# Kernel optimization log

Measured on AMD Instinct MI355X. Metric: run time of the kernel, lower is better.

Reference implementation:

```python
import jax, jax.numpy as jnp
import numpy as np

H = 256    # hidden_size
CVQ = 64   # vq_ph_channel
K = 128    # vq_ph_codebook_dim
NL = 5     # num_layers per ConvBlocks
NB = 2     # layers_in_block
KS = 3     # kernel_size


def _ln_c(x, g, b, eps=1e-5):
    # LayerNorm over channel dim of a [B, C, T] tensor
    m = jnp.mean(x, axis=1, keepdims=True)
    v = jnp.mean((x - m) ** 2, axis=1, keepdims=True)
    return (x - m) * jax.lax.rsqrt(v + eps) * g[None, :, None] + b[None, :, None]


def _causal_conv(x, w, b):
    # x [B,Cin,T], w [Cout,Cin,K]; left (causal) padding of K-1
    y = jax.lax.conv_general_dilated(x, w, (1,), [(w.shape[-1] - 1, 0)],
                                     dimension_numbers=('NCH', 'OIH', 'NCH'))
    return y + b[None, :, None]


def _pw(x, w, b):
    # pointwise (kernel-size-1) conv: w [Cout, Cin]
    return jnp.einsum('oi,bit->bot', w, x) + b[None, :, None]


def _conv_blocks(x, mask, ln_g, ln_b, w1, b1, w2, b2, last_g, last_b, post_w, post_b):
    # LeftPadConvBlocks: NL residual blocks x NB sub-blocks of
    # LN -> causal conv (C->2C, k=3) -> *k^-0.5 -> GELU -> 1x1 conv (2C->C), residual + mask
    scale = KS ** -0.5
    for i in range(NL):
        for j in range(NB):
            h = _ln_c(x, ln_g[i, j], ln_b[i, j])
            h = _causal_conv(h, w1[i, j], b1[i, j]) * scale
            h = jax.nn.gelu(h, approximate=False)
            h = _pw(h, w2[i, j], b2[i, j])
            x = (x + h) * mask
    x = _ln_c(x, last_g, last_b) * mask
    x = _causal_conv(x, post_w, post_b) * mask
    return x


def _group_by_segs(h_bct, mel2ph, L):
    # scatter-mean mel frames into phoneme segments; index 0 = padding (dropped)
    h = jnp.swapaxes(h_bct, 1, 2)  # [B, T, H]
    def one(hb, mb):
        s = jnp.zeros((L + 1, hb.shape[-1]), hb.dtype).at[mb].add(hb)
        c = jnp.zeros((L + 1,), hb.dtype).at[mb].add(1.0)
        return s[1:] / jnp.clip(c[1:], 1.0)[:, None]
    g = jax.vmap(one)(h, mel2ph)   # [B, L, H]
    return jnp.swapaxes(g, 1, 2)   # [B, H, L]


def _vq(z, codebook, beta=0.25):
    # EMA-VQ forward math: nearest-codebook lookup + straight-through + commitment loss
    x = jnp.swapaxes(z, 1, 2)                                # [B, T, C]
    d = (jnp.sum(x ** 2, -1, keepdims=True)
         - 2.0 * jnp.einsum('btc,kc->btk', x, codebook)
         + jnp.sum(codebook ** 2, -1))                       # [B, T, K]
    idx = jnp.argmin(d, axis=-1)                             # [B, T]
    q = codebook[idx]                                        # [B, T, C]
    loss = beta * jnp.mean((x - jax.lax.stop_gradient(q)) ** 2)
    q_st = x + jax.lax.stop_gradient(q - x)
    return jnp.swapaxes(q_st, 1, 2), loss, idx


def setup_inputs() -> dict:
    key = jax.random.key(0)
    ks = list(jax.random.split(key, 64))
    it = iter(ks)
    B, T, L = 16, 2048, 512
    f = lambda shape, s: jax.random.normal(next(it), shape, jnp.float32) * s
    inp = {}
    inp['x'] = jax.random.normal(next(it), (B, 80, T), jnp.float32)
    inp['in_nonpadding'] = jnp.ones((B, 1, T), jnp.float32)
    inp['in_mel2ph'] = jnp.sort(jax.random.randint(next(it), (B, T), 1, L + 1), axis=-1)
    inp['ph_nonpadding'] = jnp.ones((B, 1, L), jnp.float32)
    inp['conv_in_w'] = f((H, 80), 0.05)
    inp['conv_in_b'] = jnp.zeros((H,), jnp.float32)
    for p in ('enc', 'pn'):
        inp[p + '_ln_g'] = jnp.ones((NL, NB, H), jnp.float32)
        inp[p + '_ln_b'] = jnp.zeros((NL, NB, H), jnp.float32)
        inp[p + '_w1'] = f((NL, NB, 2 * H, H, KS), 0.03)
        inp[p + '_b1'] = jnp.zeros((NL, NB, 2 * H), jnp.float32)
        inp[p + '_w2'] = f((NL, NB, H, 2 * H), 0.03)
        inp[p + '_b2'] = jnp.zeros((NL, NB, H), jnp.float32)
        inp[p + '_last_g'] = jnp.ones((H,), jnp.float32)
        inp[p + '_last_b'] = jnp.zeros((H,), jnp.float32)
        inp[p + '_post_w'] = f((H, H, KS), 0.03)
        inp[p + '_post_b'] = jnp.zeros((H,), jnp.float32)
    inp['proj_in_w'] = f((CVQ, H), 0.05)
    inp['proj_in_b'] = jnp.zeros((CVQ,), jnp.float32)
    inp['proj_out_w'] = f((H, CVQ), 0.05)
    inp['proj_out_b'] = jnp.zeros((H,), jnp.float32)
    inp['codebook'] = f((K, CVQ), 0.1)
    return inp


def reference(x, in_nonpadding, in_mel2ph, ph_nonpadding,
              conv_in_w, conv_in_b,
              enc_ln_g, enc_ln_b, enc_w1, enc_b1, enc_w2, enc_b2,
              enc_last_g, enc_last_b, enc_post_w, enc_post_b,
              pn_ln_g, pn_ln_b, pn_w1, pn_b1, pn_w2, pn_b2,
              pn_last_g, pn_last_b, pn_post_w, pn_post_b,
              proj_in_w, proj_in_b, proj_out_w, proj_out_b, codebook):
    L = ph_nonpadding.shape[-1]
    h = _pw(x, conv_in_w, conv_in_b) * in_nonpadding                     # ph_conv_in
    h = _conv_blocks(h, in_nonpadding, enc_ln_g, enc_ln_b, enc_w1, enc_b1,
                     enc_w2, enc_b2, enc_last_g, enc_last_b,
                     enc_post_w, enc_post_b) * in_nonpadding             # ph_encoder
    h = _group_by_segs(h, in_mel2ph, L)                                  # [B, H, L]
    h = _conv_blocks(h, ph_nonpadding, pn_ln_g, pn_ln_b, pn_w1, pn_b1,
                     pn_w2, pn_b2, pn_last_g, pn_last_b,
                     pn_post_w, pn_post_b) * ph_nonpadding               # ph_postnet
    z = _pw(h, proj_in_w, proj_in_b)                                     # ph_latents_proj_in
    q, vq_loss, idx = _vq(z, codebook)                                   # VQ
    out = _pw(q, proj_out_w, proj_out_b)                                 # ph_latents_proj_out
    return out, vq_loss, idx
```

## Files before the change

kernel.cpp:

```cpp
#include <hip/hip_runtime.h>
#include <hip/hip_bf16.h>


typedef unsigned short u16;
typedef unsigned int u32;
typedef __attribute__((ext_vector_type(8))) _Float16 f16x8;
typedef __attribute__((ext_vector_type(16))) float f32x16;

#define OUT_LOSS_OFF 2097152
#define OUT_IDX_OFF  2097153

__device__ __forceinline__ void split_f16(float x, u16& h, u16& l) {
    union { _Float16 f; u16 u; } a, b;
    a.f = (_Float16)x;
    float hf = (float)a.f;
    b.f = (_Float16)(x - hf);
    h = a.u; l = b.u;
}

__global__ __launch_bounds__(256) void k_t_mat(const float* __restrict__ w,
                                               float* __restrict__ wt,
                                               int G, int O, int I) {
    size_t n = (size_t)G * O * I;
    for (size_t i = (size_t)blockIdx.x * 256 + threadIdx.x; i < n;
         i += (size_t)gridDim.x * 256) {
        int ci = (int)(i % I);
        int o  = (int)((i / I) % O);
        int g  = (int)(i / ((size_t)I * O));
        wt[((size_t)g * I + ci) * O + o] = w[i];
    }
}

__global__ __launch_bounds__(256) void k_t_w1mf(const float* __restrict__ w,
                                                u16* __restrict__ BH,
                                                u16* __restrict__ BL, int S) {
    size_t N = (size_t)S * 3 * 16 * 16 * 64 * 8;
    for (size_t i = (size_t)blockIdx.x * 256 + threadIdx.x; i < N;
         i += (size_t)gridDim.x * 256) {
        int j = (int)(i & 7); size_t r = i >> 3;
        int L = (int)(r & 63); r >>= 6;
        int nt = (int)(r & 15); r >>= 4;
        int kb = (int)(r & 15); r >>= 4;
        int k3 = (int)(r % 3); int s = (int)(r / 3);
        int oc = nt * 32 + (L & 31);
        int c = kb * 16 + ((L >> 5) << 3) + j;
        float v = w[(((size_t)s * 512 + oc) * 256 + c) * 3 + k3];
        u16 h, l; split_f16(v, h, l);
        BH[i] = h; BL[i] = l;
    }
}

__global__ __launch_bounds__(256) void k_t_w2mf(const float* __restrict__ w,
                                                u16* __restrict__ BH,
                                                u16* __restrict__ BL, int S) {
    size_t N = (size_t)S * 32 * 8 * 64 * 8;
    for (size_t i = (size_t)blockIdx.x * 256 + threadIdx.x; i < N;
         i += (size_t)gridDim.x * 256) {
        int j = (int)(i & 7);
        int L = (int)((i >> 3) & 63);
        int nt = (int)((i >> 9) & 7);
        int kb = (int)((i >> 12) & 31);
        int s = (int)(i >> 17);
        int oc = nt * 32 + (L & 31);
        int ic = kb * 16 + ((L >> 5) << 3) + j;
        float v = w[((size_t)s * 256 + oc) * 512 + ic];
        u16 h, l; split_f16(v, h, l);
        BH[i] = h; BL[i] = l;
    }
}

__global__ __launch_bounds__(256) void k_t_wpmf(const float* __restrict__ w,
                                                u16* __restrict__ BH,
                                                u16* __restrict__ BL) {
    int i = blockIdx.x * 256 + threadIdx.x;
    int j = i & 7;
    int L = (i >> 3) & 63;
    int nt = (i >> 9) & 7;
    int kb = (i >> 12) & 15;
    int k3 = i >> 16;
    int oc = nt * 32 + (L & 31);
    int c = kb * 16 + ((L >> 5) << 3) + j;
    float v = w[((size_t)oc * 256 + c) * 3 + k3];
    u16 h, l; split_f16(v, h, l);
    BH[i] = h; BL[i] = l;
}

template <int CIN, int COUT, int CHUNK, bool STATS>
__global__ __launch_bounds__(256) void k_pw(const float* __restrict__ x,
                                            const float* __restrict__ wt,
                                            const float* __restrict__ bias,
                                            const float* __restrict__ mask,
                                            float* __restrict__ y,
                                            float* __restrict__ MM,
                                            float* __restrict__ IV, int T) {
    extern __shared__ float X[];
    constexpr int NG = COUT / CHUNK;
    __shared__ float rs[64 * NG], rs2[64 * NG];
    const int b = blockIdx.y, t0 = blockIdx.x * 64;
    for (int i = threadIdx.x; i < CIN * 64; i += 256) {
        int ci = i >> 6, j = i & 63;
        X[i] = x[((size_t)b * CIN + ci) * T + t0 + j];
    }
    __syncthreads();
    const int tl = threadIdx.x & 63;
    const int g = __builtin_amdgcn_readfirstlane((int)(threadIdx.x >> 6));
    float acc[CHUNK];
#pragma unroll
    for (int o = 0; o < CHUNK; o++) acc[o] = 0.f;
    for (int i = 0; i < CIN; i++) {
        float xv = X[i * 64 + tl];
        const float* wr = wt + (size_t)i * COUT + g * CHUNK;
#pragma unroll
        for (int o = 0; o < CHUNK; o++) acc[o] = fmaf(wr[o], xv, acc[o]);
    }
    float mk = mask ? mask[(size_t)b * T + t0 + tl] : 1.0f;
    float s = 0.f, s2 = 0.f;
#pragma unroll
    for (int o = 0; o < CHUNK; o++) {
        int oc = g * CHUNK + o;
        float val = (acc[o] + bias[oc]) * mk;
        y[((size_t)b * COUT + oc) * T + t0 + tl] = val;
        s += val; s2 += val * val;
    }
    if constexpr (STATS) {
        rs[g * 64 + tl] = s; rs2[g * 64 + tl] = s2;
        __syncthreads();
        if (threadIdx.x < 64) {
            float ss = 0.f, ss2 = 0.f;
#pragma unroll
            for (int gg = 0; gg < NG; gg++) {
                ss += rs[gg * 64 + threadIdx.x];
                ss2 += rs2[gg * 64 + threadIdx.x];
            }
            float m = ss * (1.0f / COUT);
            float var = ss2 * (1.0f / COUT) - m * m;
            MM[(size_t)b * T + t0 + threadIdx.x] = m;
            IV[(size_t)b * T + t0 + threadIdx.x] = 1.0f / sqrtf(var + 1e-5f);
        }
    }
}

template <int M>
__global__ __launch_bounds__(512, (M == 32 ? 6 : 4)) void k_sub(
    const float* __restrict__ xin, float* __restrict__ xout,
    const float* __restrict__ MMi, const float* __restrict__ IVi,
    const float* __restrict__ lng, const float* __restrict__ lnb,
    const u16* __restrict__ B1H, const u16* __restrict__ B1L,
    const float* __restrict__ b1,
    const u16* __restrict__ B2H, const u16* __restrict__ B2L,
    const float* __restrict__ b2, const float* __restrict__ mask,
    float* __restrict__ MMo, float* __restrict__ IVo, int T) {
    constexpr int MT = M / 32;
    constexpr int SH = (M + 2) * 264 * 2;
    constexpr int CG = 512 / M;
    constexpr int CPT = 256 / CG;
    __shared__ __align__(16) char smem[2 * SH + 4096];
    u16* LH = (u16*)smem;
    u16* LL = (u16*)(smem + SH);
    u16* GH = (u16*)smem;
    u16* GL = (u16*)(smem + SH);
    float* SOUT = (float*)smem;
    float* rs  = (float*)(smem + 2 * SH);
    float* rs2 = (float*)(smem + 2 * SH + 2048);

    const int tid = threadIdx.x;
    const int b = blockIdx.y, t0 = blockIdx.x * M;
    const size_t xoff = (size_t)b * 256 * T;
    const size_t bT = (size_t)b * T;

    {
        int jj = tid & (M - 1);
        int cg = tid / M;
        int t = t0 - 2 + jj;
        bool ok = (t >= 0);
        float m = ok ? MMi[bT + t] : 0.f;
        float v = ok ? IVi[bT + t] : 0.f;
#pragma unroll
        for (int i = 0; i < CPT; i++) {
            int c = cg + i * CG;
            float xv = ok ? xin[xoff + (size_t)c * T + t] : 0.f;
            float ln = ok ? ((xv - m) * v * lng[c] + lnb[c]) : 0.f;
            u16 h, l; split_f16(ln, h, l);
            LH[jj * 264 + c] = h; LL[jj * 264 + c] = l;
        }
        int j2 = M + (tid >> 8);
        int c2 = tid & 255;
        int t2 = t0 + (M - 2) + (tid >> 8);
        float m2 = MMi[bT + t2], v2 = IVi[bT + t2];
        float x2 = xin[xoff + (size_t)c2 * T + t2];
        float ln2 = (x2 - m2) * v2 * lng[c2] + lnb[c2];
        u16 h2, l2; split_f16(ln2, h2, l2);
        LH[j2 * 264 + c2] = h2; LL[j2 * 264 + c2] = l2;
    }
    __syncthreads();

    const int lane = tid & 63;
    const int w = tid >> 6;
    const int arow = lane & 31;
    const int acol = (lane >> 5) << 3;
    const int thalf = (lane >> 5) << 2;
    const float ks = 0.5773502691896258f;
    const int oc_l = w * 32 + (lane & 31);
    const u16* b1h0 = B1H + (size_t)w * 512 + (size_t)lane * 8;
    const u16* b1l0 = B1L + (size_t)w * 512 + (size_t)lane * 8;
    const u16* b1h1 = B1H + (size_t)(8 + w) * 512 + (size_t)lane * 8;
    const u16* b1l1 = B1L + (size_t)(8 + w) * 512 + (size_t)lane * 8;
    const u16* b2h = B2H + (size_t)w * 512 + (size_t)lane * 8;
    const u16* b2l = B2L + (size_t)w * 512 + (size_t)lane * 8;

    f32x16 c0[MT], c1[MT];
#pragma unroll
    for (int m = 0; m < MT; m++)
#pragma unroll
        for (int r = 0; r < 16; r++) { c0[m][r] = 0.f; c1[m][r] = 0.f; }
    __builtin_amdgcn_s_setprio(1);
#pragma unroll 2
    for (int kk = 0; kk < 48; kk++) {
        int k3 = kk >> 4, kb = kk & 15;
        f16x8 bh0 = *(const f16x8*)(b1h0 + (size_t)kk * 8192);
        f16x8 bl0 = *(const f16x8*)(b1l0 + (size_t)kk * 8192);
        f16x8 bh1 = *(const f16x8*)(b1h1 + (size_t)kk * 8192);
        f16x8 bl1 = *(const f16x8*)(b1l1 + (size_t)kk * 8192);
#pragma unroll
        for (int m = 0; m < MT; m++) {
            int ao = (m * 32 + arow + k3) * 264 + kb * 16 + acol;
            f16x8 ah = *(const f16x8*)&LH[ao];
            f16x8 al = *(const f16x8*)&LL[ao];
            c0[m] = __builtin_amdgcn_mfma_f32_32x32x16_f16(ah, bh0, c0[m], 0, 0, 0);
            c1[m] = __builtin_amdgcn_mfma_f32_32x32x16_f16(ah, bh1, c1[m], 0, 0, 0);
            c0[m] = __builtin_amdgcn_mfma_f32_32x32x16_f16(ah, bl0, c0[m], 0, 0, 0);
            c1[m] = __builtin_amdgcn_mfma_f32_32x32x16_f16(ah, bl1, c1[m], 0, 0, 0);
            c0[m] = __builtin_amdgcn_mfma_f32_32x32x16_f16(al, bh0, c0[m], 0, 0, 0);
            c1[m] = __builtin_amdgcn_mfma_f32_32x32x16_f16(al, bh1, c1[m], 0, 0, 0);
        }
    }
    __builtin_amdgcn_s_setprio(0);
    __syncthreads();

    {
        float bb = b1[oc_l];
#pragma unroll
        for (int m = 0; m < MT; m++)
#pragma unroll
            for (int r = 0; r < 16; r++) {
                int trow = m * 32 + thalf + ((r >> 2) << 3) + (r & 3);
                float y = (c0[m][r] + bb) * ks;
                float ge = 0.5f * y * (1.0f + erff(y * 0.7071067811865476f));
                u16 h, l; split_f16(ge, h, l);
                GH[trow * 264 + oc_l] = h; GL[trow * 264 + oc_l] = l;
            }
    }
    __syncthreads();

    f32x16 c2acc[MT];
#pragma unroll
    for (int m = 0; m < MT; m++)
#pragma unroll
        for (int r = 0; r < 16; r++) c2acc[m][r] = 0.f;
    __builtin_amdgcn_s_setprio(1);
#pragma unroll 2
    for (int i = 0; i < 16; i++) {
        f16x8 bh2 = *(const f16x8*)(b2h + (size_t)i * 4096);
        f16x8 bl2 = *(const f16x8*)(b2l + (size_t)i * 4096);
#pragma unroll
        for (int m = 0; m < MT; m++) {
            int go = (m * 32 + arow) * 264 + i * 16 + acol;
            f16x8 gh = *(const f16x8*)&GH[go];
            f16x8 gl = *(const f16x8*)&GL[go];
            c2acc[m] = __builtin_amdgcn_mfma_f32_32x32x16_f16(gh, bh2, c2acc[m], 0, 0, 0);
            c2acc[m] = __builtin_amdgcn_mfma_f32_32x32x16_f16(gh, bl2, c2acc[m], 0, 0, 0);
            c2acc[m] = __builtin_amdgcn_mfma_f32_32x32x16_f16(gl, bh2, c2acc[m], 0, 0, 0);
        }
    }
    __builtin_amdgcn_s_setprio(0);
    __syncthreads();

    {
        float bb = b1[256 + oc_l];
#pragma unroll
        for (int m = 0; m < MT; m++)
#pragma unroll
            for (int r = 0; r < 16; r++) {
                int trow = m * 32 + thalf + ((r >> 2) << 3) + (r & 3);
                float y = (c1[m][r] + bb) * ks;
                float ge = 0.5f * y * (1.0f + erff(y * 0.7071067811865476f));
                u16 h, l; split_f16(ge, h, l);
                GH[trow * 264 + oc_l] = h; GL[trow * 264 + oc_l] = l;
            }
    }
    __syncthreads();

    __builtin_amdgcn_s_setprio(1);
#pragma unroll 2
    for (int i = 0; i < 16; i++) {
        f16x8 bh2 = *(const f16x8*)(b2h + (size_t)(16 + i) * 4096);
        f16x8 bl2 = *(const f16x8*)(b2l + (size_t)(16 + i) * 4096);
#pragma unroll
        for (int m = 0; m < MT; m++) {
            int go = (m * 32 + arow) * 264 + i * 16 + acol;
            f16x8 gh = *(const f16x8*)&GH[go];
            f16x8 gl = *(const f16x8*)&GL[go];
            c2acc[m] = __builtin_amdgcn_mfma_f32_32x32x16_f16(gh, bh2, c2acc[m], 0, 0, 0);
            c2acc[m] = __builtin_amdgcn_mfma_f32_32x32x16_f16(gh, bl2, c2acc[m], 0, 0, 0);
            c2acc[m] = __builtin_amdgcn_mfma_f32_32x32x16_f16(gl, bh2, c2acc[m], 0, 0, 0);
        }
    }
    __builtin_amdgcn_s_setprio(0);
    __syncthreads();

#pragma unroll
    for (int m = 0; m < MT; m++)
#pragma unroll
        for (int r = 0; r < 16; r++) {
            int trow = m * 32 + thalf + ((r >> 2) << 3) + (r & 3);
            SOUT[trow * 260 + oc_l] = c2acc[m][r];
        }
    __syncthreads();
    {
        int t = tid & (M - 1), cg = tid / M;
        float mk = mask[bT + t0 + t];
        float s = 0.f, s2 = 0.f;
#pragma unroll
        for (int i = 0; i < CPT; i++) {
            int c = cg * CPT + i;
            size_t adr = xoff + (size_t)c * T + t0 + t;
            float val = (xin[adr] + SOUT[t * 260 + c] + b2[c]) * mk;
            xout[adr] = val;
            s += val; s2 += val * val;
        }
        rs[tid] = s; rs2[tid] = s2;
    }
    __syncthreads();
    if (tid < M) {
        float ss = 0.f, ss2 = 0.f;
#pragma unroll
        for (int k = 0; k < CG; k++) {
            ss += rs[k * M + tid]; ss2 += rs2[k * M + tid];
        }
        float m = ss * (1.0f / 256.0f);
        float var = ss2 * (1.0f / 256.0f) - m * m;
        MMo[bT + t0 + tid] = m;
        IVo[bT + t0 + tid] = 1.0f / sqrtf(var + 1e-5f);
    }
}

template <int M>
__global__ __launch_bounds__(512, (M == 32 ? 8 : 4)) void k_lnc(
    const float* __restrict__ xin, float* __restrict__ xout,
    const float* __restrict__ MM, const float* __restrict__ IV,
    const float* __restrict__ lg, const float* __restrict__ lb,
    const u16* __restrict__ BH, const u16* __restrict__ BL,
    const float* __restrict__ bias, const float* __restrict__ mask, int T) {
    constexpr int MT = M / 32;
    constexpr int SH = (M + 2) * 264 * 2;
    constexpr int CG = 512 / M;
    constexpr int CPT = 256 / CG;
    __shared__ __align__(16) char smem[2 * SH];
    u16* LH = (u16*)smem;
    u16* LL = (u16*)(smem + SH);
    float* SOUT = (float*)smem;

    const int tid = threadIdx.x;
    const int b = blockIdx.y, t0 = blockIdx.x * M;
    const size_t xoff = (size_t)b * 256 * T;
    const size_t bT = (size_t)b * T;

    {
        int jj = tid & (M - 1);
        int cg = tid / M;
        int t = t0 - 2 + jj;
        bool ok = (t >= 0);
        float m = ok ? MM[bT + t] : 0.f;
        float v = ok ? IV[bT + t] : 0.f;
        float mk = ok ? mask[bT + t] : 0.f;
#pragma unroll
        for (int i = 0; i < CPT; i++) {
            int c = cg + i * CG;
            float xv = ok ? xin[xoff + (size_t)c * T + t] : 0.f;
            float ln = ok ? ((xv - m) * v * lg[c] + lb[c]) * mk : 0.f;
            u16 h, l; split_f16(ln, h, l);
            LH[jj * 264 + c] = h; LL[jj * 264 + c] = l;
        }
        int j2 = M + (tid >> 8);
        int c2 = tid & 255;
        int t2 = t0 + (M - 2) + (tid >> 8);
        float ln2 = ((xin[xoff + (size_t)c2 * T + t2] - MM[bT + t2]) *
                     IV[bT + t2] * lg[c2] + lb[c2]) * mask[bT + t2];
        u16 h2, l2; split_f16(ln2, h2, l2);
        LH[j2 * 264 + c2] = h2; LL[j2 * 264 + c2] = l2;
    }
    __syncthreads();

    const int lane = tid & 63;
    const int w = tid >> 6;
    const int arow = lane & 31;
    const int acol = (lane >> 5) << 3;
    const int thalf = (lane >> 5) << 2;
    const u16* bph = BH + (size_t)w * 512 + (size_t)lane * 8;
    const u16* bpl = BL + (size_t)w * 512 + (size_t)lane * 8;

    f32x16 aH[MT], aM[MT];
#pragma unroll
    for (int m = 0; m < MT; m++)
#pragma unroll
        for (int r = 0; r < 16; r++) { aH[m][r] = 0.f; aM[m][r] = 0.f; }
    __builtin_amdgcn_s_setprio(1);
#pragma unroll 2
    for (int kk = 0; kk < 48; kk++) {
        int k3 = kk >> 4, kb = kk & 15;
        f16x8 bh = *(const f16x8*)(bph + (size_t)kk * 4096);
        f16x8 bl = *(const f16x8*)(bpl + (size_t)kk * 4096);
#pragma unroll
        for (int m = 0; m < MT; m++) {
            int ao = (m * 32 + arow + k3) * 264 + kb * 16 + acol;
            f16x8 ah = *(const f16x8*)&LH[ao];
            f16x8 al = *(const f16x8*)&LL[ao];
            aH[m] = __builtin_amdgcn_mfma_f32_32x32x16_f16(ah, bh, aH[m], 0, 0, 0);
            aM[m] = __builtin_amdgcn_mfma_f32_32x32x16_f16(ah, bl, aM[m], 0, 0, 0);
            aM[m] = __builtin_amdgcn_mfma_f32_32x32x16_f16(al, bh, aM[m], 0, 0, 0);
        }
    }
    __builtin_amdgcn_s_setprio(0);
    __syncthreads();
    {
        int oc = w * 32 + (lane & 31);
#pragma unroll
        for (int m = 0; m < MT; m++)
#pragma unroll
            for (int r = 0; r < 16; r++) {
                int trow = m * 32 + thalf + ((r >> 2) << 3) + (r & 3);
                SOUT[trow * 260 + oc] = aH[m][r] + aM[m][r];
            }
    }
    __syncthreads();
    {
        int t = tid & (M - 1), cg = tid / M;
        float mk = mask[bT + t0 + t];
#pragma unroll
        for (int i = 0; i < CPT; i++) {
            int c = cg * CPT + i;
            xout[xoff + (size_t)c * T + t0 + t] =
                (SOUT[t * 260 + c] + bias[c]) * mk;
        }
    }
}

__global__ __launch_bounds__(256) void k_counts(const int* __restrict__ m2p,
                                                int* __restrict__ cnt) {
    __shared__ int c[512];
    int b = blockIdx.x;
    for (int i = threadIdx.x; i < 512; i += 256) c[i] = 0;
    __syncthreads();
    for (int t = threadIdx.x; t < 2048; t += 256) {
        int p = m2p[b * 2048 + t];
        if (p >= 1 && p <= 512) atomicAdd(&c[p - 1], 1);
    }
    __syncthreads();
    for (int i = threadIdx.x; i < 512; i += 256) cnt[b * 512 + i] = c[i];
}

__global__ __launch_bounds__(256) void k_scatter(const float* __restrict__ h,
                                                 const int* __restrict__ m2p,
                                                 float* __restrict__ g) {
    extern __shared__ float sm[];
    float* HT = sm;
    int* ph = (int*)(sm + 256 * 65);
    int b = blockIdx.y, t0 = blockIdx.x * 64;
    if (threadIdx.x < 64) ph[threadIdx.x] = m2p[b * 2048 + t0 + threadIdx.x];
    for (int i = threadIdx.x; i < 256 * 64; i += 256) {
        int c = i >> 6, j = i & 63;
        HT[c * 65 + j] = h[((size_t)b * 256 + c) * 2048 + t0 + j];
    }
    __syncthreads();
    int c = threadIdx.x;
    float run = 0.f;
    int cur = ph[0];
    for (int j = 0; j < 64; j++) {
        int p = ph[j];
        if (p != cur) {
            if (cur >= 1 && cur <= 512)
                atomicAdd(&g[((size_t)b * 256 + c) * 512 + cur - 1], run);
            run = 0.f;
            cur = p;
        }
        run += HT[c * 65 + j];
    }
    if (cur >= 1 && cur <= 512)
        atomicAdd(&g[((size_t)b * 256 + c) * 512 + cur - 1], run);
}

__global__ __launch_bounds__(512) void k_postprep(float* __restrict__ g,
                                                  const int* __restrict__ cnt,
                                                  float* __restrict__ MM,
                                                  float* __restrict__ IV) {
    int b = blockIdx.x, l = threadIdx.x;
    int c1 = cnt[b * 512 + l];
    if (c1 < 1) c1 = 1;
    float rc = 1.0f / (float)c1;
    float s = 0.f, s2 = 0.f;
    for (int c = 0; c < 256; c++) {
        size_t idx = ((size_t)b * 256 + c) * 512 + l;
        float v = g[idx] * rc;
        g[idx] = v;
        s += v; s2 += v * v;
    }
    float m = s * (1.0f / 256.0f);
    float var = s2 * (1.0f / 256.0f) - m * m;
    MM[(size_t)b * 512 + l] = m;
    IV[(size_t)b * 512 + l] = 1.0f / sqrtf(var + 1e-5f);
}

__global__ __launch_bounds__(256) void k_vq(const float* __restrict__ z,
                                            const float* __restrict__ cb,
                                            int* __restrict__ idxout,
                                            float* __restrict__ out,
                                            float* __restrict__ lossacc) {
    int n = blockIdx.x * 256 + threadIdx.x;
    int b = n >> 9, l = n & 511;
    float zr[64];
#pragma unroll
    for (int c = 0; c < 64; c++) zr[c] = z[((size_t)b * 64 + c) * 512 + l];
    float best = 3.4e38f;
    int bi = 0;
    for (int k = 0; k < 128; k++) {
        const float* cr = cb + k * 64;
        float d = 0.f;
#pragma unroll
        for (int c = 0; c < 64; c++) {
            float t = zr[c] - cr[c];
            d = fmaf(t, t, d);
        }
        if (d < best) { best = d; bi = k; }
    }
    idxout[n] = bi;
    out[OUT_IDX_OFF + n] = (float)bi;
    atomicAdd(lossacc, best);
}

__global__ void k_loss(const float* __restrict__ acc, float* __restrict__ out) {
    if (threadIdx.x == 0 && blockIdx.x == 0)
        out[OUT_LOSS_OFF] = 0.25f * acc[0] * (1.0f / 524288.0f);
}

__global__ __launch_bounds__(256) void k_projout(const float* __restrict__ cb,
                                                 const int* __restrict__ idx,
                                                 const float* __restrict__ wt,
                                                 const float* __restrict__ bias,
                                                 float* __restrict__ out) {
    __shared__ float Q[64 * 64];
    __shared__ int ids[64];
    int b = blockIdx.y, l0 = blockIdx.x * 64;
    if (threadIdx.x < 64) ids[threadIdx.x] = idx[b * 512 + l0 + threadIdx.x];
    __syncthreads();
    for (int i = threadIdx.x; i < 4096; i += 256) {
        int c = i >> 6, l = i & 63;
        Q[c * 64 + l] = cb[ids[l] * 64 + c];
    }
    __syncthreads();
    int tl = threadIdx.x & 63;
    int g = __builtin_amdgcn_readfirstlane((int)(threadIdx.x >> 6));
    float acc[64];
#pragma unroll
    for (int o = 0; o < 64; o++) acc[o] = 0.f;
    for (int i = 0; i < 64; i++) {
        float xv = Q[i * 64 + tl];
        const float* wr = wt + i * 256 + g * 64;
#pragma unroll
        for (int o = 0; o < 64; o++) acc[o] = fmaf(wr[o], xv, acc[o]);
    }
#pragma unroll
    for (int o = 0; o < 64; o++) {
        int oc = g * 64 + o;
        out[(size_t)b * 131072 + (size_t)oc * 512 + l0 + tl] = acc[o] + bias[oc];
    }
}

extern "C" void kernel_launch(void* const* d_in, const int* in_sizes, int n_in,
                              void* d_out, int out_size, void* d_ws, size_t ws_size,
                              hipStream_t stream) {
    (void)in_sizes; (void)n_in; (void)out_size; (void)ws_size;
    const float* x          = (const float*)d_in[0];
    const float* in_np      = (const float*)d_in[1];
    const int*   mel2ph     = (const int*)d_in[2];
    const float* ph_np      = (const float*)d_in[3];
    const float* conv_in_w  = (const float*)d_in[4];
    const float* conv_in_b  = (const float*)d_in[5];
    const float* e_ln_g = (const float*)d_in[6];
    const float* e_ln_b = (const float*)d_in[7];
    const float* e_w1   = (const float*)d_in[8];
    const float* e_b1   = (const float*)d_in[9];
    const float* e_w2   = (const float*)d_in[10];
    const float* e_b2   = (const float*)d_in[11];
    const float* e_lg   = (const float*)d_in[12];
    const float* e_lb   = (const float*)d_in[13];
    const float* e_pw   = (const float*)d_in[14];
    const float* e_pb   = (const float*)d_in[15];
    const float* p_ln_g = (const float*)d_in[16];
    const float* p_ln_b = (const float*)d_in[17];
    const float* p_w1   = (const float*)d_in[18];
    const float* p_b1   = (const float*)d_in[19];
    const float* p_w2   = (const float*)d_in[20];
    const float* p_b2   = (const float*)d_in[21];
    const float* p_lg   = (const float*)d_in[22];
    const float* p_lb   = (const float*)d_in[23];
    const float* p_pw   = (const float*)d_in[24];
    const float* p_pb   = (const float*)d_in[25];
    const float* proj_in_w  = (const float*)d_in[26];
    const float* proj_in_b  = (const float*)d_in[27];
    const float* proj_out_w = (const float*)d_in[28];
    const float* proj_out_b = (const float*)d_in[29];
    const float* codebook   = (const float*)d_in[30];
    float* out = (float*)d_out;

    float* ws = (float*)d_ws;
    float* A      = ws;
    float* Bb     = A + 8388608;
    float* CINT   = Bb + 8388608;
    float* PINT   = CINT + 20480;
    float* POUTT  = PINT + 16384;
    float* Z      = POUTT + 16384;
    float* MM0    = Z + 524288;
    float* IV0    = MM0 + 32768;
    float* MM1    = IV0 + 32768;
    float* IV1    = MM1 + 32768;
    int*   CNT    = (int*)(IV1 + 32768);
    int*   IDX    = CNT + 8192;
    float* LOSS   = (float*)(IDX + 8192);
    u16*   BH1E   = (u16*)(LOSS + 64);
    u16*   BL1E   = BH1E + 3932160;
    u16*   BH1P   = BL1E + 3932160;
    u16*   BL1P   = BH1P + 3932160;
    u16*   BH2E   = BL1P + 3932160;
    u16*   BL2E   = BH2E + 1310720;
    u16*   BH2P   = BL2E + 1310720;
    u16*   BL2P   = BH2P + 1310720;
    u16*   PH_E   = BL2P + 1310720;
    u16*   PL_E   = PH_E + 196608;
    u16*   PH_P   = PL_E + 196608;
    u16*   PL_P   = PH_P + 196608;

    k_t_w1mf<<<dim3(4096), dim3(256), 0, stream>>>(e_w1, BH1E, BL1E, 10);
    k_t_w1mf<<<dim3(4096), dim3(256), 0, stream>>>(p_w1, BH1P, BL1P, 10);
    k_t_w2mf<<<dim3(2048), dim3(256), 0, stream>>>(e_w2, BH2E, BL2E, 10);
    k_t_w2mf<<<dim3(2048), dim3(256), 0, stream>>>(p_w2, BH2P, BL2P, 10);
    k_t_wpmf<<<dim3(768),  dim3(256), 0, stream>>>(e_pw, PH_E, PL_E);
    k_t_wpmf<<<dim3(768),  dim3(256), 0, stream>>>(p_pw, PH_P, PL_P);
    k_t_mat  <<<dim3(80),  dim3(256), 0, stream>>>(conv_in_w, CINT, 1, 256, 80);
    k_t_mat  <<<dim3(64),  dim3(256), 0, stream>>>(proj_in_w, PINT, 1, 64, 256);
    k_t_mat  <<<dim3(64),  dim3(256), 0, stream>>>(proj_out_w, POUTT, 1, 256, 64);

    const size_t sm_scat = 256 * 65 * sizeof(float) + 64 * sizeof(int);

    k_pw<80, 256, 64, true><<<dim3(32, 16), dim3(256), 80 * 64 * 4, stream>>>(
        x, CINT, conv_in_b, in_np, A, MM0, IV0, 2048);

    float* cur = A;
    float* nxt = Bb;
    for (int s = 0; s < 10; s++) {
        float* mi = (s & 1) ? MM1 : MM0;
        float* vi = (s & 1) ? IV1 : IV0;
        float* mo = (s & 1) ? MM0 : MM1;
        float* vo = (s & 1) ? IV0 : IV1;
        k_sub<64><<<dim3(32, 16), dim3(512), 0, stream>>>(
            cur, nxt, mi, vi, e_ln_g + s * 256, e_ln_b + s * 256,
            BH1E + (size_t)s * 393216, BL1E + (size_t)s * 393216, e_b1 + s * 512,
            BH2E + (size_t)s * 131072, BL2E + (size_t)s * 131072, e_b2 + s * 256,
            in_np, mo, vo, 2048);
        float* t = cur; cur = nxt; nxt = t;
    }
    k_lnc<64><<<dim3(32, 16), dim3(512), 0, stream>>>(
        cur, nxt, MM0, IV0, e_lg, e_lb, PH_E, PL_E, e_pb, in_np, 2048);

    hipMemsetAsync(A, 0, (size_t)2097152 * 4, stream);
    hipMemsetAsync(LOSS, 0, 4, stream);
    k_counts<<<dim3(16), dim3(256), 0, stream>>>(mel2ph, CNT);
    k_scatter<<<dim3(32, 16), dim3(256), sm_scat, stream>>>(Bb, mel2ph, A);
    k_postprep<<<dim3(16), dim3(512), 0, stream>>>(A, CNT, MM0, IV0);

    cur = A; nxt = Bb;
    for (int s = 0; s < 10; s++) {
        float* mi = (s & 1) ? MM1 : MM0;
        float* vi = (s & 1) ? IV1 : IV0;
        float* mo = (s & 1) ? MM0 : MM1;
        float* vo = (s & 1) ? IV0 : IV1;
        k_sub<32><<<dim3(16, 16), dim3(512), 0, stream>>>(
            cur, nxt, mi, vi, p_ln_g + s * 256, p_ln_b + s * 256,
            BH1P + (size_t)s * 393216, BL1P + (size_t)s * 393216, p_b1 + s * 512,
            BH2P + (size_t)s * 131072, BL2P + (size_t)s * 131072, p_b2 + s * 256,
            ph_np, mo, vo, 512);
        float* t = cur; cur = nxt; nxt = t;
    }
    k_lnc<32><<<dim3(16, 16), dim3(512), 0, stream>>>(
        cur, nxt, MM0, IV0, p_lg, p_lb, PH_P, PL_P, p_pb, ph_np, 512);

    k_pw<256, 64, 16, false><<<dim3(8, 16), dim3(256), 256 * 64 * 4, stream>>>(
        Bb, PINT, proj_in_b, nullptr, Z, nullptr, nullptr, 512);

    k_vq<<<dim3(32), dim3(256), 0, stream>>>(Z, codebook, IDX, out, LOSS);
    k_loss<<<dim3(1), dim3(64), 0, stream>>>(LOSS, out);
    k_projout<<<dim3(8, 16), dim3(256), 0, stream>>>(codebook, IDX, POUTT,
                                                     proj_out_b, out);
}
```

Baseline: 2.274 ms.

## Use 1024-thread sub-block kernel splitting conv output channels across 16 waves

Adds a k_sub16 kernel for the postnet stage (T=512) that runs 1024 threads per block. Each of 16 waves computes one 32-channel slice of the 512-channel causal conv, instead of 8 waves each covering two slices. The upper half of the GELU output is held in registers and written to LDS only after the first half of the 1x1 conv has consumed it. This raises per-block parallelism for the small 256-block grid, at the cost of extra barriers and idle waves during the second GEMM. The generic k_sub also reuses its c0 accumulator for the second GEMM and uses a uniform occupancy hint, which is meant to reduce register pressure.

```diff
diff --git a/kernel.cpp b/kernel.cpp
--- a/kernel.cpp
+++ b/kernel.cpp
@@ -141,7 +141,7 @@
 }
 
 template <int M>
-__global__ __launch_bounds__(512, (M == 32 ? 6 : 4)) void k_sub(
+__global__ __launch_bounds__(512, 4) void k_sub(
     const float* __restrict__ xin, float* __restrict__ xout,
     const float* __restrict__ MMi, const float* __restrict__ IVi,
     const float* __restrict__ lng, const float* __restrict__ lnb,
@@ -252,11 +252,10 @@
     }
     __syncthreads();
 
-    f32x16 c2acc[MT];
 #pragma unroll
     for (int m = 0; m < MT; m++)
 #pragma unroll
-        for (int r = 0; r < 16; r++) c2acc[m][r] = 0.f;
+        for (int r = 0; r < 16; r++) c0[m][r] = 0.f;
     __builtin_amdgcn_s_setprio(1);
 #pragma unroll 2
     for (int i = 0; i < 16; i++) {
@@ -267,9 +266,9 @@
             int go = (m * 32 + arow) * 264 + i * 16 + acol;
             f16x8 gh = *(const f16x8*)&GH[go];
             f16x8 gl = *(const f16x8*)&GL[go];
-            c2acc[m] = __builtin_amdgcn_mfma_f32_32x32x16_f16(gh, bh2, c2acc[m], 0, 0, 0);
-            c2acc[m] = __builtin_amdgcn_mfma_f32_32x32x16_f16(gh, bl2, c2acc[m], 0, 0, 0);
-            c2acc[m] = __builtin_amdgcn_mfma_f32_32x32x16_f16(gl, bh2, c2acc[m], 0, 0, 0);
+            c0[m] = __builtin_amdgcn_mfma_f32_32x32x16_f16(gh, bh2, c0[m], 0, 0, 0);
+            c0[m] = __builtin_amdgcn_mfma_f32_32x32x16_f16(gh, bl2, c0[m], 0, 0, 0);
+            c0[m] = __builtin_amdgcn_mfma_f32_32x32x16_f16(gl, bh2, c0[m], 0, 0, 0);
         }
     }
     __builtin_amdgcn_s_setprio(0);
@@ -300,9 +299,9 @@
             int go = (m * 32 + arow) * 264 + i * 16 + acol;
             f16x8 gh = *(const f16x8*)&GH[go];
             f16x8 gl = *(const f16x8*)&GL[go];
-            c2acc[m] = __builtin_amdgcn_mfma_f32_32x32x16_f16(gh, bh2, c2acc[m], 0, 0, 0);
-            c2acc[m] = __builtin_amdgcn_mfma_f32_32x32x16_f16(gh, bl2, c2acc[m], 0, 0, 0);
-            c2acc[m] = __builtin_amdgcn_mfma_f32_32x32x16_f16(gl, bh2, c2acc[m], 0, 0, 0);
+            c0[m] = __builtin_amdgcn_mfma_f32_32x32x16_f16(gh, bh2, c0[m], 0, 0, 0);
+            c0[m] = __builtin_amdgcn_mfma_f32_32x32x16_f16(gh, bl2, c0[m], 0, 0, 0);
+            c0[m] = __builtin_amdgcn_mfma_f32_32x32x16_f16(gl, bh2, c0[m], 0, 0, 0);
         }
     }
     __builtin_amdgcn_s_setprio(0);
@@ -313,7 +312,7 @@
 #pragma unroll
         for (int r = 0; r < 16; r++) {
             int trow = m * 32 + thalf + ((r >> 2) << 3) + (r & 3);
-            SOUT[trow * 260 + oc_l] = c2acc[m][r];
+            SOUT[trow * 260 + oc_l] = c0[m][r];
         }
     __syncthreads();
     {
@@ -336,6 +335,194 @@
 #pragma unroll
         for (int k = 0; k < CG; k++) {
             ss += rs[k * M + tid]; ss2 += rs2[k * M + tid];
+        }
+        float m = ss * (1.0f / 256.0f);
+        float var = ss2 * (1.0f / 256.0f) - m * m;
+        MMo[bT + t0 + tid] = m;
+        IVo[bT + t0 + tid] = 1.0f / sqrtf(var + 1e-5f);
+    }
+}
+
+__global__ __launch_bounds__(1024, 4) void k_sub16(
+    const float* __restrict__ xin, float* __restrict__ xout,
+    const float* __restrict__ MMi, const float* __restrict__ IVi,
+    const float* __restrict__ lng, const float* __restrict__ lnb,
+    const u16* __restrict__ B1H, const u16* __restrict__ B1L,
+    const float* __restrict__ b1,
+    const u16* __restrict__ B2H, const u16* __restrict__ B2L,
+    const float* __restrict__ b2, const float* __restrict__ mask,
+    float* __restrict__ MMo, float* __restrict__ IVo, int T) {
+    __shared__ __align__(16) char smem[44096];
+    u16* LH = (u16*)smem;
+    u16* LL = (u16*)(smem + 17952);
+    u16* GH = (u16*)smem;
+    u16* GL = (u16*)(smem + 17952);
+    float* SOUT = (float*)smem;
+    float* rs  = (float*)(smem + 35904);
+    float* rs2 = (float*)(smem + 40000);
+
+    const int tid = threadIdx.x;
+    const int b = blockIdx.y, t0 = blockIdx.x * 32;
+    const size_t xoff = (size_t)b * 256 * T;
+    const size_t bT = (size_t)b * T;
+
+    {
+        int jj = tid & 31;
+        int cg = tid >> 5;
+        int t = t0 - 2 + jj;
+        bool ok = (t >= 0);
+        float m = ok ? MMi[bT + t] : 0.f;
+        float v = ok ? IVi[bT + t] : 0.f;
+#pragma unroll
+        for (int i = 0; i < 8; i++) {
+            int c = cg + i * 32;
+            float xv = ok ? xin[xoff + (size_t)c * T + t] : 0.f;
+            float ln = ok ? ((xv - m) * v * lng[c] + lnb[c]) : 0.f;
+            u16 h, l; split_f16(ln, h, l);
+            LH[jj * 264 + c] = h; LL[jj * 264 + c] = l;
+        }
+        if (tid < 512) {
+            int j2 = 32 + (tid >> 8);
+            int c2 = tid & 255;
+            int t2 = t0 + 30 + (tid >> 8);
+            float ln2 = (xin[xoff + (size_t)c2 * T + t2] - MMi[bT + t2]) *
+                        IVi[bT + t2] * lng[c2] + lnb[c2];
+            u16 h2, l2; split_f16(ln2, h2, l2);
+            LH[j2 * 264 + c2] = h2; LL[j2 * 264 + c2] = l2;
+        }
+    }
+    __syncthreads();
+
+    const int lane = tid & 63;
+    const int w = tid >> 6;
+    const int arow = lane & 31;
+    const int acol = (lane >> 5) << 3;
+    const int thalf = (lane >> 5) << 2;
+    const float ks = 0.5773502691896258f;
+    const int oc_l = w * 32 + (lane & 31);
+    const u16* b1h = B1H + (size_t)w * 512 + (size_t)lane * 8;
+    const u16* b1l = B1L + (size_t)w * 512 + (size_t)lane * 8;
+
+    f32x16 cc;
+#pragma unroll
+    for (int r = 0; r < 16; r++) cc[r] = 0.f;
+    __builtin_amdgcn_s_setprio(1);
+#pragma unroll 4
+    for (int kk = 0; kk < 48; kk++) {
+        int k3 = kk >> 4, kb = kk & 15;
+        int ao = (arow + k3) * 264 + kb * 16 + acol;
+        f16x8 ah = *(const f16x8*)&LH[ao];
+        f16x8 al = *(const f16x8*)&LL[ao];
+        f16x8 bh = *(const f16x8*)(b1h + (size_t)kk * 8192);
+        f16x8 bl = *(const f16x8*)(b1l + (size_t)kk * 8192);
+        cc = __builtin_amdgcn_mfma_f32_32x32x16_f16(ah, bh, cc, 0, 0, 0);
+        cc = __builtin_amdgcn_mfma_f32_32x32x16_f16(ah, bl, cc, 0, 0, 0);
+        cc = __builtin_amdgcn_mfma_f32_32x32x16_f16(al, bh, cc, 0, 0, 0);
+    }
+    __builtin_amdgcn_s_setprio(0);
+    __syncthreads();
+
+    u32 preg[16];
+    {
+        float bb = b1[oc_l];
+        if (w < 8) {
+#pragma unroll
+            for (int r = 0; r < 16; r++) {
+                int trow = thalf + ((r >> 2) << 3) + (r & 3);
+                float y = (cc[r] + bb) * ks;
+                float ge = 0.5f * y * (1.0f + erff(y * 0.7071067811865476f));
+                u16 h, l; split_f16(ge, h, l);
+                GH[trow * 264 + oc_l] = h; GL[trow * 264 + oc_l] = l;
+            }
+        } else {
+#pragma unroll
+            for (int r = 0; r < 16; r++) {
+                float y = (cc[r] + bb) * ks;
+                float ge = 0.5f * y * (1.0f + erff(y * 0.7071067811865476f));
+                u16 h, l; split_f16(ge, h, l);
+                preg[r] = ((u32)h << 16) | (u32)l;
+            }
+        }
+    }
+    __syncthreads();
+
+    const u16* b2h = B2H + (size_t)(w & 7) * 512 + (size_t)lane * 8;
+    const u16* b2l = B2L + (size_t)(w & 7) * 512 + (size_t)lane * 8;
+    if (w < 8) {
+#pragma unroll
+        for (int r = 0; r < 16; r++) cc[r] = 0.f;
+        __builtin_amdgcn_s_setprio(1);
+#pragma unroll 2
+        for (int i = 0; i < 16; i++) {
+            int go = arow * 264 + i * 16 + acol;
+            f16x8 gh = *(const f16x8*)&GH[go];
+            f16x8 gl = *(const f16x8*)&GL[go];
+            f16x8 bh2 = *(const f16x8*)(b2h + (size_t)i * 4096);
+            f16x8 bl2 = *(const f16x8*)(b2l + (size_t)i * 4096);
+            cc = __builtin_amdgcn_mfma_f32_32x32x16_f16(gh, bh2, cc, 0, 0, 0);
+            cc = __builtin_amdgcn_mfma_f32_32x32x16_f16(gh, bl2, cc, 0, 0, 0);
+            cc = __builtin_amdgcn_mfma_f32_32x32x16_f16(gl, bh2, cc, 0, 0, 0);
+        }
+        __builtin_amdgcn_s_setprio(0);
+    }
+    __syncthreads();
+
+    if (w >= 8) {
+        int col = oc_l - 256;
+#pragma unroll
+        for (int r = 0; r < 16; r++) {
+            int trow = thalf + ((r >> 2) << 3) + (r & 3);
+            GH[trow * 264 + col] = (u16)(preg[r] >> 16);
+            GL[trow * 264 + col] = (u16)(preg[r] & 0xffff);
+        }
+    }
+    __syncthreads();
+
+    if (w < 8) {
+        __builtin_amdgcn_s_setprio(1);
+#pragma unroll 2
+        for (int i = 0; i < 16; i++) {
+            int go = arow * 264 + i * 16 + acol;
+            f16x8 gh = *(const f16x8*)&GH[go];
+            f16x8 gl = *(const f16x8*)&GL[go];
+            f16x8 bh2 = *(const f16x8*)(b2h + (size_t)(16 + i) * 4096);
+            f16x8 bl2 = *(const f16x8*)(b2l + (size_t)(16 + i) * 4096);
+            cc = __builtin_amdgcn_mfma_f32_32x32x16_f16(gh, bh2, cc, 0, 0, 0);
+            cc = __builtin_amdgcn_mfma_f32_32x32x16_f16(gh, bl2, cc, 0, 0, 0);
+            cc = __builtin_amdgcn_mfma_f32_32x32x16_f16(gl, bh2, cc, 0, 0, 0);
+        }
+        __builtin_amdgcn_s_setprio(0);
+    }
+    __syncthreads();
+
+    if (w < 8) {
+#pragma unroll
+        for (int r = 0; r < 16; r++) {
+            int trow = thalf + ((r >> 2) << 3) + (r & 3);
+            SOUT[trow * 260 + oc_l] = cc[r];
+        }
+    }
+    __syncthreads();
+    {
+        int t = tid & 31, cg = tid >> 5;
+        float mk = mask[bT + t0 + t];
+        float s = 0.f, s2 = 0.f;
+#pragma unroll
+        for (int i = 0; i < 8; i++) {
+            int c = cg * 8 + i;
+            size_t adr = xoff + (size_t)c * T + t0 + t;
+            float val = (xin[adr] + SOUT[t * 260 + c] + b2[c]) * mk;
+            xout[adr] = val;
+            s += val; s2 += val * val;
+        }
+        rs[tid] = s; rs2[tid] = s2;
+    }
+    __syncthreads();
+    if (tid < 32) {
+        float ss = 0.f, ss2 = 0.f;
+#pragma unroll
+        for (int k = 0; k < 32; k++) {
+            ss += rs[k * 32 + tid]; ss2 += rs2[k * 32 + tid];
         }
         float m = ss * (1.0f / 256.0f);
         float var = ss2 * (1.0f / 256.0f) - m * m;
@@ -683,7 +870,7 @@
         float* vi = (s & 1) ? IV1 : IV0;
         float* mo = (s & 1) ? MM0 : MM1;
         float* vo = (s & 1) ? IV0 : IV1;
-        k_sub<32><<<dim3(16, 16), dim3(512), 0, stream>>>(
+        k_sub16<<<dim3(16, 16), dim3(1024), 0, stream>>>(
             cur, nxt, mi, vi, p_ln_g + s * 256, p_ln_b + s * 256,
             BH1P + (size_t)s * 393216, BL1P + (size_t)s * 393216, p_b1 + s * 512,
             BH2P + (size_t)s * 131072, BL2P + (size_t)s * 131072, p_b2 + s * 256,
```

After: 2.119 ms. 6.8% less time.
